# Kernel tuning notes

Hardware: AMD Instinct MI355X
Metric: run time of the kernel (lower is better)

## Reference

```python
import jax, jax.numpy as jnp
import numpy as np

B, T, C, HS = 8, 4096, 1024, 128
BLOCK = 4096  # block_size; T == BLOCK here


def _pyr_mask(bs):
    # Faithful numpy translation of the torch 'pyr' buffer construction.
    h = bs // 2
    top = np.repeat(np.flip(np.tril(np.ones((h, h), np.float32)), axis=1), 2, axis=0)  # (bs, h)
    reps = np.array([2] * (h - 1) + [1])
    bot = np.concatenate(
        [np.zeros((1, h), np.float32),
         np.repeat(np.tril(np.ones((h, h), np.float32)), reps, axis=0)], axis=0)  # (bs, h)
    return np.concatenate([top, bot], axis=1)  # (bs, bs)


def setup_inputs() -> dict:
    key = jax.random.key(0)
    kx, kq, kk, kv = jax.random.split(key, 4)
    s = C ** -0.5
    x = jax.random.normal(kx, (B, T, C), jnp.float32)
    Wq = jax.random.normal(kq, (C, HS), jnp.float32) * s
    Wk = jax.random.normal(kk, (C, HS), jnp.float32) * s
    Wv = jax.random.normal(kv, (C, HS), jnp.float32) * s
    return {"x": x, "Wq": Wq, "Wk": Wk, "Wv": Wv}


def reference(x, Wq, Wk, Wv):
    Tlen = x.shape[1]
    start = (BLOCK - Tlen) // 2
    end = BLOCK + (-(BLOCK - Tlen)) // 2  # python floor-div, matches torch slicing
    mask = jnp.asarray(_pyr_mask(BLOCK)[:Tlen, start:end])  # (T, T) 0/1

    q = x @ Wq  # (B, T, HS)
    k = x @ Wk
    v = x @ Wv
    wei = jnp.einsum('btd,bsd->bts', q, k) * (HS ** -0.5)  # (B, T, T)
    wei = jnp.where(mask == 0, -jnp.inf, wei)  # bidirectional_mode == 'bi'
    wei = jax.nn.softmax(wei, axis=-1)
    # dropout p=0.0 -> identity
    return wei @ v  # (B, T, HS)
```

## Files before the change

kernel.cpp:

```cpp
#include <hip/hip_runtime.h>

typedef unsigned short u16;
typedef __attribute__((ext_vector_type(8))) short bf16x8;
typedef __attribute__((ext_vector_type(8))) unsigned short u16x8;
typedef __attribute__((ext_vector_type(4))) float f32x4;
typedef __attribute__((ext_vector_type(4))) unsigned short u16x4;

#define Bn 8
#define Tn 4096
#define Cn 1024
#define HSn 128

__device__ __forceinline__ float bf2f(u16 b) {
    unsigned u = ((unsigned)b) << 16;
    return __builtin_bit_cast(float, u);
}
__device__ __forceinline__ u16 f2bf(float f) {
    unsigned u = __builtin_bit_cast(unsigned, f);
    unsigned r = (u + 0x7fffu + ((u >> 16) & 1u)) >> 16;
    return (u16)r;
}

extern "C" __global__ __launch_bounds__(256) void head_wtrans(
    const float* __restrict__ Wq, const float* __restrict__ Wk,
    const float* __restrict__ Wv, u16* __restrict__ wt) {
    const float* W = (blockIdx.y == 0) ? Wq : (blockIdx.y == 1) ? Wk : Wv;
    const float scale =
        (blockIdx.y == 0) ? (0.08838834764831845f * 1.4426950408889634f) : 1.0f;
    u16* o = wt + (size_t)blockIdx.y * Cn * HSn;
    int tid = blockIdx.x * 256 + threadIdx.x;
    int n = tid >> 10, kk = tid & 1023;
    o[tid] = f2bf(W[kk * HSn + n] * scale);
}

extern "C" __global__ __launch_bounds__(256, 2) void head_proj(
    const float* __restrict__ x, const u16* __restrict__ wt, u16* __restrict__ qo,
    u16* __restrict__ ko, u16* __restrict__ vto) {
    __shared__ __align__(16) u16 aL[128 * 40];
    __shared__ __align__(16) u16 bL[128 * 40];
    const int tid = threadIdx.x;
    const int w = tid >> 6, l = tid & 63, quad = l >> 4, ln = l & 15;
    const int bm0 = blockIdx.x * 128;
    const int ws = blockIdx.y;
    const u16* wtw = wt + (size_t)ws * Cn * HSn;

    const f32x4 zero4 = {0.f, 0.f, 0.f, 0.f};
    f32x4 acc[4][4];
#pragma unroll
    for (int i = 0; i < 4; i++)
#pragma unroll
        for (int j = 0; j < 4; j++) acc[i][j] = zero4;

    const int m0w = (w & 1) * 64, n0w = (w >> 1) * 64;

    for (int kt = 0; kt < Cn / 32; kt++) {
        __syncthreads();
#pragma unroll
        for (int p = 0; p < 4; p++) {
            int idx = p * 256 + tid;
            int row = idx >> 3, ch = idx & 7;
            f32x4 va = *(const f32x4*)(x + ((size_t)(bm0 + row)) * Cn + kt * 32 + ch * 4);
            u16x4 vb;
#pragma unroll
            for (int j = 0; j < 4; j++) vb[j] = f2bf(va[j]);
            *(u16x4*)(aL + row * 40 + ch * 4) = vb;
        }
#pragma unroll
        for (int p = 0; p < 2; p++) {
            int idx = p * 256 + tid;
            int row = idx >> 2, ch = idx & 3;
            u16x8 vb = *(const u16x8*)(wtw + (size_t)row * Cn + kt * 32 + ch * 8);
            *(u16x8*)(bL + row * 40 + ch * 8) = vb;
        }
        __syncthreads();
        bf16x8 af[4], bf[4];
#pragma unroll
        for (int mi = 0; mi < 4; mi++) {
            int R = m0w + mi * 16 + ln;
            af[mi] = *(const bf16x8*)(aL + R * 40 + quad * 8);
        }
#pragma unroll
        for (int ni = 0; ni < 4; ni++) {
            int R = n0w + ni * 16 + ln;
            bf[ni] = *(const bf16x8*)(bL + R * 40 + quad * 8);
        }
#pragma unroll
        for (int mi = 0; mi < 4; mi++)
#pragma unroll
            for (int ni = 0; ni < 4; ni++)
                acc[mi][ni] = __builtin_amdgcn_mfma_f32_16x16x32_bf16(
                    af[mi], bf[ni], acc[mi][ni], 0, 0, 0);
    }
    if (ws == 2) {
#pragma unroll
        for (int mi = 0; mi < 4; mi++)
#pragma unroll
            for (int ni = 0; ni < 4; ni++)
#pragma unroll
                for (int r = 0; r < 4; r++) {
                    int grow = bm0 + m0w + mi * 16 + quad * 4 + r;
                    int bb = grow >> 12, t = grow & 4095;
                    int col = n0w + ni * 16 + ln;
                    vto[((size_t)bb * HSn + col) * Tn + t] = f2bf(acc[mi][ni][r]);
                }
    } else {
        u16* out = (ws == 0) ? qo : ko;
#pragma unroll
        for (int mi = 0; mi < 4; mi++)
#pragma unroll
            for (int ni = 0; ni < 4; ni++)
#pragma unroll
                for (int r = 0; r < 4; r++) {
                    int grow = bm0 + m0w + mi * 16 + quad * 4 + r;
                    int col = n0w + ni * 16 + ln;
                    out[(size_t)grow * HSn + col] = f2bf(acc[mi][ni][r]);
                }
    }
}

extern "C" __global__ __launch_bounds__(256) void head_flash(
    const u16* __restrict__ q, const u16* __restrict__ k, const u16* __restrict__ vt,
    float* __restrict__ out) {
    __shared__ __align__(16) u16 kL[64 * 136];
    __shared__ __align__(16) u16 vL[128 * 72];
    __shared__ __align__(16) u16 pL[4 * 16 * 72];
    const int tid = threadIdx.x;
    const int w = tid >> 6, l = tid & 63, quad = l >> 4, ln = l & 15;
    const int b = blockIdx.y;
    const int bx = blockIdx.x;

    const int rkBase = tid >> 4, ckK = tid & 15;
    const int rvBase = tid >> 3, ckV = tid & 7;

    for (int phase = 0; phase < 2; phase++) {
        const int qb = phase == 0 ? 63 - bx : bx;
        const int q0 = qb * 64;
        const int qrow = q0 + w * 16;

        bf16x8 qf[4];
#pragma unroll
        for (int ks = 0; ks < 4; ks++)
            qf[ks] = *(const bf16x8*)(q + ((size_t)b * Tn + qrow + ln) * HSn + ks * 32 +
                                      quad * 8);

        const f32x4 zero4 = {0.f, 0.f, 0.f, 0.f};
        float m2[4], l2[4];
        f32x4 o[8];
#pragma unroll
        for (int r = 0; r < 4; r++) {
            m2[r] = -1e30f;
            l2[r] = 0.f;
        }
#pragma unroll
        for (int dt = 0; dt < 8; dt++) o[dt] = zero4;

        const int qmax = q0 + 63;
        const int tlo = (2047 - (qmax >> 1)) >> 6;
        const int thi = (2047 + ((qmax + 1) >> 1)) >> 6;

        u16x8 pk[4], pv[4];
        {
            const int t0 = tlo * 64;
#pragma unroll
            for (int p = 0; p < 4; p++)
                pk[p] = *(const u16x8*)(k + ((size_t)b * Tn + t0 + p * 16 + rkBase) * HSn +
                                        ckK * 8);
#pragma unroll
            for (int p = 0; p < 4; p++)
                pv[p] = *(const u16x8*)(vt + ((size_t)b * HSn + p * 32 + rvBase) * Tn +
                                        t0 + ckV * 8);
        }

        for (int kt = tlo; kt <= thi; kt++) {
            const int t0 = kt * 64;
            __syncthreads();
#pragma unroll
            for (int p = 0; p < 4; p++)
                *(u16x8*)(kL + (p * 16 + rkBase) * 136 + ckK * 8) = pk[p];
#pragma unroll
            for (int p = 0; p < 4; p++)
                *(u16x8*)(vL + (p * 32 + rvBase) * 72 + ckV * 8) = pv[p];
            if (kt < thi) {
                const int t1 = t0 + 64;
#pragma unroll
                for (int p = 0; p < 4; p++)
                    pk[p] = *(const u16x8*)(k + ((size_t)b * Tn + t1 + p * 16 + rkBase) *
                                                    HSn + ckK * 8);
#pragma unroll
                for (int p = 0; p < 4; p++)
                    pv[p] = *(const u16x8*)(vt + ((size_t)b * HSn + p * 32 + rvBase) * Tn +
                                            t1 + ckV * 8);
            }
            __syncthreads();

            f32x4 s[4];
#pragma unroll
            for (int nt = 0; nt < 4; nt++) s[nt] = zero4;
#pragma unroll
            for (int nt = 0; nt < 4; nt++) {
                int R = nt * 16 + ln;
#pragma unroll
                for (int ks = 0; ks < 4; ks++) {
                    bf16x8 kf = *(const bf16x8*)(kL + R * 136 + (ks * 4 + quad) * 8);
                    s[nt] =
                        __builtin_amdgcn_mfma_f32_16x16x32_bf16(qf[ks], kf, s[nt], 0, 0, 0);
                }
            }
#pragma unroll
            for (int nt = 0; nt < 4; nt++)
#pragma unroll
                for (int r = 0; r < 4; r++) {
                    int qa = qrow + quad * 4 + r;
                    int c = t0 + nt * 16 + ln;
                    bool valid = (c >= 2047 - (qa >> 1)) && (c <= 2047 + ((qa + 1) >> 1));
                    s[nt][r] = valid ? s[nt][r] : -1e30f;
                }
            float mc[4];
#pragma unroll
            for (int r = 0; r < 4; r++) {
                float m = fmaxf(fmaxf(s[0][r], s[1][r]), fmaxf(s[2][r], s[3][r]));
#pragma unroll
                for (int off = 1; off < 16; off <<= 1)
                    m = fmaxf(m, __shfl_xor(m, off, 64));
                mc[r] = m;
            }
            float alpha[4], mn[4], ls[4];
#pragma unroll
            for (int r = 0; r < 4; r++) {
                mn[r] = fmaxf(m2[r], mc[r]);
                alpha[r] = exp2f(m2[r] - mn[r]);
                m2[r] = mn[r];
                ls[r] = 0.f;
            }
#pragma unroll
            for (int nt = 0; nt < 4; nt++)
#pragma unroll
                for (int r = 0; r < 4; r++) {
                    float pv2 = exp2f(s[nt][r] - mn[r]);
                    u16 pb = f2bf(pv2);
                    ls[r] += bf2f(pb);
                    pL[w * 1152 + (quad * 4 + r) * 72 + nt * 16 + ln] = pb;
                }
#pragma unroll
            for (int r = 0; r < 4; r++) {
                float t = ls[r];
#pragma unroll
                for (int off = 1; off < 16; off <<= 1) t += __shfl_xor(t, off, 64);
                l2[r] = l2[r] * alpha[r] + t;
            }
#pragma unroll
            for (int dt = 0; dt < 8; dt++) {
                f32x4 oo = o[dt];
#pragma unroll
                for (int r = 0; r < 4; r++) oo[r] *= alpha[r];
                o[dt] = oo;
            }
#pragma unroll
            for (int jt = 0; jt < 2; jt++) {
                bf16x8 pf = *(const bf16x8*)(pL + w * 1152 + ln * 72 + jt * 32 + quad * 8);
#pragma unroll
                for (int dt = 0; dt < 8; dt++) {
                    int R = dt * 16 + ln;
                    bf16x8 vf = *(const bf16x8*)(vL + R * 72 + (jt * 4 + quad) * 8);
                    o[dt] = __builtin_amdgcn_mfma_f32_16x16x32_bf16(pf, vf, o[dt], 0, 0, 0);
                }
            }
        }
        float rl[4];
#pragma unroll
        for (int r = 0; r < 4; r++) rl[r] = 1.0f / l2[r];
#pragma unroll
        for (int dt = 0; dt < 8; dt++)
#pragma unroll
            for (int r = 0; r < 4; r++) {
                int row = qrow + quad * 4 + r;
                out[((size_t)b * Tn + row) * HSn + dt * 16 + ln] = o[dt][r] * rl[r];
            }
    }
}

extern "C" void kernel_launch(void* const* d_in, const int* in_sizes, int n_in,
                              void* d_out, int out_size, void* d_ws, size_t ws_size,
                              hipStream_t stream) {
    const float* x = (const float*)d_in[0];
    const float* Wq = (const float*)d_in[1];
    const float* Wk = (const float*)d_in[2];
    const float* Wv = (const float*)d_in[3];
    float* outp = (float*)d_out;
    char* ws = (char*)d_ws;
    u16* wt = (u16*)(ws);
    u16* qb = (u16*)(ws + (1u << 20));
    u16* kb = (u16*)(ws + (9u << 20));
    u16* vtb = (u16*)(ws + (17u << 20));

    head_wtrans<<<dim3(512, 3), 256, 0, stream>>>(Wq, Wk, Wv, wt);
    head_proj<<<dim3(256, 3), 256, 0, stream>>>(x, wt, qb, kb, vtb);
    head_flash<<<dim3(32, 8), 256, 0, stream>>>(qb, kb, vtb, outp);
}
```

Baseline: 366.8 us.

## Fuse QKV projection into one pass and split flash attention grid

The projection kernel now computes Q, K and V in a single block per row tile, so x is read and converted to bf16 once instead of three times. Global loads are register-prefetched one k-step ahead. The flash kernel drops the two-phase loop in favour of a 512-block grid with one query tile per block. It also computes S transposed (K as the A operand), so row max and sum reductions need two cross-lane shuffles instead of four per row. The costs are higher register pressure in the projection (three accumulator sets, occupancy bound of 1) and only 256 projection blocks.

After: 347.6 us. 5.2% less time.

```diff
diff --git a/kernel.cpp b/kernel.cpp
--- a/kernel.cpp
+++ b/kernel.cpp
@@ -33,89 +33,102 @@
     o[tid] = f2bf(W[kk * HSn + n] * scale);
 }
 
-extern "C" __global__ __launch_bounds__(256, 2) void head_proj(
+extern "C" __global__ __launch_bounds__(256, 1) void head_proj(
     const float* __restrict__ x, const u16* __restrict__ wt, u16* __restrict__ qo,
     u16* __restrict__ ko, u16* __restrict__ vto) {
     __shared__ __align__(16) u16 aL[128 * 40];
-    __shared__ __align__(16) u16 bL[128 * 40];
+    __shared__ __align__(16) u16 bL[3 * 128 * 40];
     const int tid = threadIdx.x;
     const int w = tid >> 6, l = tid & 63, quad = l >> 4, ln = l & 15;
     const int bm0 = blockIdx.x * 128;
-    const int ws = blockIdx.y;
-    const u16* wtw = wt + (size_t)ws * Cn * HSn;
 
     const f32x4 zero4 = {0.f, 0.f, 0.f, 0.f};
-    f32x4 acc[4][4];
-#pragma unroll
-    for (int i = 0; i < 4; i++)
-#pragma unroll
-        for (int j = 0; j < 4; j++) acc[i][j] = zero4;
+    f32x4 acc[3][4][4];
+#pragma unroll
+    for (int s = 0; s < 3; s++)
+#pragma unroll
+        for (int i = 0; i < 4; i++)
+#pragma unroll
+            for (int j = 0; j < 4; j++) acc[s][i][j] = zero4;
 
     const int m0w = (w & 1) * 64, n0w = (w >> 1) * 64;
+
+    f32x4 xp[4];
+    u16x8 wp[3][2];
+    const int xrow[4] = {tid >> 3, (256 + tid) >> 3, (512 + tid) >> 3, (768 + tid) >> 3};
+    const int xch = tid & 7;
+    const int wrow[2] = {tid >> 2, (256 + tid) >> 2};
+    const int wch = tid & 3;
+
+#pragma unroll
+    for (int p = 0; p < 4; p++)
+        xp[p] = *(const f32x4*)(x + ((size_t)(bm0 + xrow[p])) * Cn + xch * 4);
+#pragma unroll
+    for (int s = 0; s < 3; s++)
+#pragma unroll
+        for (int p = 0; p < 2; p++)
+            wp[s][p] = *(const u16x8*)(wt + (size_t)s * Cn * HSn + (size_t)wrow[p] * Cn +
+                                       wch * 8);
 
     for (int kt = 0; kt < Cn / 32; kt++) {
         __syncthreads();
 #pragma unroll
         for (int p = 0; p < 4; p++) {
-            int idx = p * 256 + tid;
-            int row = idx >> 3, ch = idx & 7;
-            f32x4 va = *(const f32x4*)(x + ((size_t)(bm0 + row)) * Cn + kt * 32 + ch * 4);
             u16x4 vb;
 #pragma unroll
-            for (int j = 0; j < 4; j++) vb[j] = f2bf(va[j]);
-            *(u16x4*)(aL + row * 40 + ch * 4) = vb;
-        }
-#pragma unroll
-        for (int p = 0; p < 2; p++) {
-            int idx = p * 256 + tid;
-            int row = idx >> 2, ch = idx & 3;
-            u16x8 vb = *(const u16x8*)(wtw + (size_t)row * Cn + kt * 32 + ch * 8);
-            *(u16x8*)(bL + row * 40 + ch * 8) = vb;
+            for (int j = 0; j < 4; j++) vb[j] = f2bf(xp[p][j]);
+            *(u16x4*)(aL + xrow[p] * 40 + xch * 4) = vb;
+        }
+#pragma unroll
+        for (int s = 0; s < 3; s++)
+#pragma unroll
+            for (int p = 0; p < 2; p++)
+                *(u16x8*)(bL + s * 5120 + wrow[p] * 40 + wch * 8) = wp[s][p];
+        if (kt + 1 < Cn / 32) {
+            const int kn = (kt + 1) * 32;
+#pragma unroll
+            for (int p = 0; p < 4; p++)
+                xp[p] = *(const f32x4*)(x + ((size_t)(bm0 + xrow[p])) * Cn + kn + xch * 4);
+#pragma unroll
+            for (int s = 0; s < 3; s++)
+#pragma unroll
+                for (int p = 0; p < 2; p++)
+                    wp[s][p] = *(const u16x8*)(wt + (size_t)s * Cn * HSn +
+                                               (size_t)wrow[p] * Cn + kn + wch * 8);
         }
         __syncthreads();
-        bf16x8 af[4], bf[4];
-#pragma unroll
-        for (int mi = 0; mi < 4; mi++) {
-            int R = m0w + mi * 16 + ln;
-            af[mi] = *(const bf16x8*)(aL + R * 40 + quad * 8);
-        }
-#pragma unroll
-        for (int ni = 0; ni < 4; ni++) {
-            int R = n0w + ni * 16 + ln;
-            bf[ni] = *(const bf16x8*)(bL + R * 40 + quad * 8);
-        }
+        bf16x8 af[4];
 #pragma unroll
         for (int mi = 0; mi < 4; mi++)
+            af[mi] = *(const bf16x8*)(aL + (m0w + mi * 16 + ln) * 40 + quad * 8);
+#pragma unroll
+        for (int s = 0; s < 3; s++) {
+            bf16x8 bf[4];
 #pragma unroll
             for (int ni = 0; ni < 4; ni++)
-                acc[mi][ni] = __builtin_amdgcn_mfma_f32_16x16x32_bf16(
-                    af[mi], bf[ni], acc[mi][ni], 0, 0, 0);
+                bf[ni] =
+                    *(const bf16x8*)(bL + s * 5120 + (n0w + ni * 16 + ln) * 40 + quad * 8);
+#pragma unroll
+            for (int mi = 0; mi < 4; mi++)
+#pragma unroll
+                for (int ni = 0; ni < 4; ni++)
+                    acc[s][mi][ni] = __builtin_amdgcn_mfma_f32_16x16x32_bf16(
+                        af[mi], bf[ni], acc[s][mi][ni], 0, 0, 0);
+        }
     }
-    if (ws == 2) {
-#pragma unroll
-        for (int mi = 0; mi < 4; mi++)
-#pragma unroll
-            for (int ni = 0; ni < 4; ni++)
-#pragma unroll
-                for (int r = 0; r < 4; r++) {
-                    int grow = bm0 + m0w + mi * 16 + quad * 4 + r;
-                    int bb = grow >> 12, t = grow & 4095;
-                    int col = n0w + ni * 16 + ln;
-                    vto[((size_t)bb * HSn + col) * Tn + t] = f2bf(acc[mi][ni][r]);
-                }
-    } else {
-        u16* out = (ws == 0) ? qo : ko;
-#pragma unroll
-        for (int mi = 0; mi < 4; mi++)
-#pragma unroll
-            for (int ni = 0; ni < 4; ni++)
-#pragma unroll
-                for (int r = 0; r < 4; r++) {
-                    int grow = bm0 + m0w + mi * 16 + quad * 4 + r;
-                    int col = n0w + ni * 16 + ln;
-                    out[(size_t)grow * HSn + col] = f2bf(acc[mi][ni][r]);
-                }
-    }
+#pragma unroll
+    for (int mi = 0; mi < 4; mi++)
+#pragma unroll
+        for (int ni = 0; ni < 4; ni++)
+#pragma unroll
+            for (int r = 0; r < 4; r++) {
+                int grow = bm0 + m0w + mi * 16 + quad * 4 + r;
+                int col = n0w + ni * 16 + ln;
+                qo[(size_t)grow * HSn + col] = f2bf(acc[0][mi][ni][r]);
+                ko[(size_t)grow * HSn + col] = f2bf(acc[1][mi][ni][r]);
+                int bb = grow >> 12, t = grow & 4095;
+                vto[((size_t)bb * HSn + col) * Tn + t] = f2bf(acc[2][mi][ni][r]);
+            }
 }
 
 extern "C" __global__ __launch_bounds__(256) void head_flash(
@@ -126,157 +139,147 @@
     __shared__ __align__(16) u16 pL[4 * 16 * 72];
     const int tid = threadIdx.x;
     const int w = tid >> 6, l = tid & 63, quad = l >> 4, ln = l & 15;
-    const int b = blockIdx.y;
     const int bx = blockIdx.x;
+    const int half = bx >> 8, idx = bx & 255;
+    const int p5 = idx & 31, b = idx >> 5;
+    const int qb = half ? p5 : 63 - p5;
+    const int q0 = qb * 64;
+    const int qrow = q0 + w * 16;
 
     const int rkBase = tid >> 4, ckK = tid & 15;
     const int rvBase = tid >> 3, ckV = tid & 7;
 
-    for (int phase = 0; phase < 2; phase++) {
-        const int qb = phase == 0 ? 63 - bx : bx;
-        const int q0 = qb * 64;
-        const int qrow = q0 + w * 16;
-
-        bf16x8 qf[4];
-#pragma unroll
-        for (int ks = 0; ks < 4; ks++)
-            qf[ks] = *(const bf16x8*)(q + ((size_t)b * Tn + qrow + ln) * HSn + ks * 32 +
-                                      quad * 8);
-
-        const f32x4 zero4 = {0.f, 0.f, 0.f, 0.f};
-        float m2[4], l2[4];
-        f32x4 o[8];
-#pragma unroll
-        for (int r = 0; r < 4; r++) {
-            m2[r] = -1e30f;
-            l2[r] = 0.f;
-        }
-#pragma unroll
-        for (int dt = 0; dt < 8; dt++) o[dt] = zero4;
-
-        const int qmax = q0 + 63;
-        const int tlo = (2047 - (qmax >> 1)) >> 6;
-        const int thi = (2047 + ((qmax + 1) >> 1)) >> 6;
-
-        u16x8 pk[4], pv[4];
-        {
-            const int t0 = tlo * 64;
+    bf16x8 qf[4];
+#pragma unroll
+    for (int ks = 0; ks < 4; ks++)
+        qf[ks] = *(const bf16x8*)(q + ((size_t)b * Tn + qrow + ln) * HSn + ks * 32 +
+                                  quad * 8);
+
+    const f32x4 zero4 = {0.f, 0.f, 0.f, 0.f};
+    float m2 = -1e30f, l2 = 0.f;
+    const int qme = qrow + ln;
+    const int clo = 2047 - (qme >> 1), chi = 2047 + ((qme + 1) >> 1);
+    f32x4 o[8];
+#pragma unroll
+    for (int dt = 0; dt < 8; dt++) o[dt] = zero4;
+
+    const int qmax = q0 + 63;
+    const int tlo = (2047 - (qmax >> 1)) >> 6;
+    const int thi = (2047 + ((qmax + 1) >> 1)) >> 6;
+
+    u16x8 pk[4], pv[4];
+    {
+        const int t0 = tlo * 64;
+#pragma unroll
+        for (int p = 0; p < 4; p++)
+            pk[p] = *(const u16x8*)(k + ((size_t)b * Tn + t0 + p * 16 + rkBase) * HSn +
+                                    ckK * 8);
+#pragma unroll
+        for (int p = 0; p < 4; p++)
+            pv[p] = *(const u16x8*)(vt + ((size_t)b * HSn + p * 32 + rvBase) * Tn + t0 +
+                                    ckV * 8);
+    }
+
+    for (int kt = tlo; kt <= thi; kt++) {
+        const int t0 = kt * 64;
+        __syncthreads();
+#pragma unroll
+        for (int p = 0; p < 4; p++)
+            *(u16x8*)(kL + (p * 16 + rkBase) * 136 + ckK * 8) = pk[p];
+#pragma unroll
+        for (int p = 0; p < 4; p++)
+            *(u16x8*)(vL + (p * 32 + rvBase) * 72 + ckV * 8) = pv[p];
+        if (kt < thi) {
+            const int t1 = t0 + 64;
 #pragma unroll
             for (int p = 0; p < 4; p++)
-                pk[p] = *(const u16x8*)(k + ((size_t)b * Tn + t0 + p * 16 + rkBase) * HSn +
+                pk[p] = *(const u16x8*)(k + ((size_t)b * Tn + t1 + p * 16 + rkBase) * HSn +
                                         ckK * 8);
 #pragma unroll
             for (int p = 0; p < 4; p++)
                 pv[p] = *(const u16x8*)(vt + ((size_t)b * HSn + p * 32 + rvBase) * Tn +
-                                        t0 + ckV * 8);
-        }
-
-        for (int kt = tlo; kt <= thi; kt++) {
-            const int t0 = kt * 64;
-            __syncthreads();
-#pragma unroll
-            for (int p = 0; p < 4; p++)
-                *(u16x8*)(kL + (p * 16 + rkBase) * 136 + ckK * 8) = pk[p];
-#pragma unroll
-            for (int p = 0; p < 4; p++)
-                *(u16x8*)(vL + (p * 32 + rvBase) * 72 + ckV * 8) = pv[p];
-            if (kt < thi) {
-                const int t1 = t0 + 64;
-#pragma unroll
-                for (int p = 0; p < 4; p++)
-                    pk[p] = *(const u16x8*)(k + ((size_t)b * Tn + t1 + p * 16 + rkBase) *
-                                                    HSn + ckK * 8);
-#pragma unroll
-                for (int p = 0; p < 4; p++)
-                    pv[p] = *(const u16x8*)(vt + ((size_t)b * HSn + p * 32 + rvBase) * Tn +
-                                            t1 + ckV * 8);
-            }
-            __syncthreads();
-
-            f32x4 s[4];
-#pragma unroll
-            for (int nt = 0; nt < 4; nt++) s[nt] = zero4;
-#pragma unroll
-            for (int nt = 0; nt < 4; nt++) {
-                int R = nt * 16 + ln;
-#pragma unroll
-                for (int ks = 0; ks < 4; ks++) {
-                    bf16x8 kf = *(const bf16x8*)(kL + R * 136 + (ks * 4 + quad) * 8);
-                    s[nt] =
-                        __builtin_amdgcn_mfma_f32_16x16x32_bf16(qf[ks], kf, s[nt], 0, 0, 0);
-                }
-            }
-#pragma unroll
-            for (int nt = 0; nt < 4; nt++)
-#pragma unroll
-                for (int r = 0; r < 4; r++) {
-                    int qa = qrow + quad * 4 + r;
-                    int c = t0 + nt * 16 + ln;
-                    bool valid = (c >= 2047 - (qa >> 1)) && (c <= 2047 + ((qa + 1) >> 1));
-                    s[nt][r] = valid ? s[nt][r] : -1e30f;
-                }
-            float mc[4];
+                                        t1 + ckV * 8);
+        }
+        __syncthreads();
+
+        f32x4 s[4];
+#pragma unroll
+        for (int nt = 0; nt < 4; nt++) s[nt] = zero4;
+#pragma unroll
+        for (int nt = 0; nt < 4; nt++) {
+            int R = nt * 16 + ln;
+#pragma unroll
+            for (int ks = 0; ks < 4; ks++) {
+                bf16x8 kf = *(const bf16x8*)(kL + R * 136 + (ks * 4 + quad) * 8);
+                s[nt] = __builtin_amdgcn_mfma_f32_16x16x32_bf16(kf, qf[ks], s[nt], 0, 0, 0);
+            }
+        }
+#pragma unroll
+        for (int nt = 0; nt < 4; nt++)
 #pragma unroll
             for (int r = 0; r < 4; r++) {
-                float m = fmaxf(fmaxf(s[0][r], s[1][r]), fmaxf(s[2][r], s[3][r]));
-#pragma unroll
-                for (int off = 1; off < 16; off <<= 1)
-                    m = fmaxf(m, __shfl_xor(m, off, 64));
-                mc[r] = m;
-            }
-            float alpha[4], mn[4], ls[4];
+                int t = t0 + nt * 16 + quad * 4 + r;
+                bool valid = (t >= clo) && (t <= chi);
+                s[nt][r] = valid ? s[nt][r] : -1e30f;
+            }
+        float mc = s[0][0];
+#pragma unroll
+        for (int nt = 0; nt < 4; nt++)
+#pragma unroll
+            for (int r = 0; r < 4; r++) mc = fmaxf(mc, s[nt][r]);
+        mc = fmaxf(mc, __shfl_xor(mc, 16, 64));
+        mc = fmaxf(mc, __shfl_xor(mc, 32, 64));
+        float mn = fmaxf(m2, mc);
+        float alpha = exp2f(m2 - mn);
+        m2 = mn;
+        float ls = 0.f;
+#pragma unroll
+        for (int nt = 0; nt < 4; nt++) {
+            u16x4 pb4;
 #pragma unroll
             for (int r = 0; r < 4; r++) {
-                mn[r] = fmaxf(m2[r], mc[r]);
-                alpha[r] = exp2f(m2[r] - mn[r]);
-                m2[r] = mn[r];
-                ls[r] = 0.f;
-            }
-#pragma unroll
-            for (int nt = 0; nt < 4; nt++)
-#pragma unroll
-                for (int r = 0; r < 4; r++) {
-                    float pv2 = exp2f(s[nt][r] - mn[r]);
-                    u16 pb = f2bf(pv2);
-                    ls[r] += bf2f(pb);
-                    pL[w * 1152 + (quad * 4 + r) * 72 + nt * 16 + ln] = pb;
-                }
-#pragma unroll
-            for (int r = 0; r < 4; r++) {
-                float t = ls[r];
-#pragma unroll
-                for (int off = 1; off < 16; off <<= 1) t += __shfl_xor(t, off, 64);
-                l2[r] = l2[r] * alpha[r] + t;
-            }
+                float pvx = exp2f(s[nt][r] - mn);
+                u16 pb = f2bf(pvx);
+                ls += bf2f(pb);
+                pb4[r] = pb;
+            }
+            *(u16x4*)(pL + w * 1152 + ln * 72 + nt * 16 + quad * 4) = pb4;
+        }
+        ls += __shfl_xor(ls, 16, 64);
+        ls += __shfl_xor(ls, 32, 64);
+        l2 = l2 * alpha + ls;
+        float aR[4];
+#pragma unroll
+        for (int r = 0; r < 4; r++) aR[r] = __shfl(alpha, quad * 4 + r, 64);
+#pragma unroll
+        for (int dt = 0; dt < 8; dt++) {
+            f32x4 oo = o[dt];
+#pragma unroll
+            for (int r = 0; r < 4; r++) oo[r] *= aR[r];
+            o[dt] = oo;
+        }
+#pragma unroll
+        for (int jt = 0; jt < 2; jt++) {
+            bf16x8 pf = *(const bf16x8*)(pL + w * 1152 + ln * 72 + jt * 32 + quad * 8);
 #pragma unroll
             for (int dt = 0; dt < 8; dt++) {
-                f32x4 oo = o[dt];
-#pragma unroll
-                for (int r = 0; r < 4; r++) oo[r] *= alpha[r];
-                o[dt] = oo;
-            }
-#pragma unroll
-            for (int jt = 0; jt < 2; jt++) {
-                bf16x8 pf = *(const bf16x8*)(pL + w * 1152 + ln * 72 + jt * 32 + quad * 8);
-#pragma unroll
-                for (int dt = 0; dt < 8; dt++) {
-                    int R = dt * 16 + ln;
-                    bf16x8 vf = *(const bf16x8*)(vL + R * 72 + (jt * 4 + quad) * 8);
-                    o[dt] = __builtin_amdgcn_mfma_f32_16x16x32_bf16(pf, vf, o[dt], 0, 0, 0);
-                }
-            }
-        }
-        float rl[4];
-#pragma unroll
-        for (int r = 0; r < 4; r++) rl[r] = 1.0f / l2[r];
-#pragma unroll
-        for (int dt = 0; dt < 8; dt++)
-#pragma unroll
-            for (int r = 0; r < 4; r++) {
-                int row = qrow + quad * 4 + r;
-                out[((size_t)b * Tn + row) * HSn + dt * 16 + ln] = o[dt][r] * rl[r];
-            }
+                int R = dt * 16 + ln;
+                bf16x8 vf = *(const bf16x8*)(vL + R * 72 + (jt * 4 + quad) * 8);
+                o[dt] = __builtin_amdgcn_mfma_f32_16x16x32_bf16(pf, vf, o[dt], 0, 0, 0);
+            }
+        }
     }
+    float inv = 1.0f / l2;
+    float rl[4];
+#pragma unroll
+    for (int r = 0; r < 4; r++) rl[r] = __shfl(inv, quad * 4 + r, 64);
+#pragma unroll
+    for (int dt = 0; dt < 8; dt++)
+#pragma unroll
+        for (int r = 0; r < 4; r++) {
+            int row = qrow + quad * 4 + r;
+            out[((size_t)b * Tn + row) * HSn + dt * 16 + ln] = o[dt][r] * rl[r];
+        }
 }
 
 extern "C" void kernel_launch(void* const* d_in, const int* in_sizes, int n_in,
@@ -294,6 +297,6 @@
     u16* vtb = (u16*)(ws + (17u << 20));
 
     head_wtrans<<<dim3(512, 3), 256, 0, stream>>>(Wq, Wk, Wv, wt);
-    head_proj<<<dim3(256, 3), 256, 0, stream>>>(x, wt, qb, kb, vtb);
-    head_flash<<<dim3(32, 8), 256, 0, stream>>>(qb, kb, vtb, outp);
-}
+    head_proj<<<dim3(256), 256, 0, stream>>>(x, wt, qb, kb, vtb);
+    head_flash<<<dim3(512), 256, 0, stream>>>(qb, kb, vtb, outp);
+}
```
